# Optimization experiments

Measured on AMD Instinct MI355X. Metric: run time of the kernel, lower is better.

Reference implementation:

```python
import jax, jax.numpy as jnp
import numpy as np

B, L, E, H = 4, 2048, 512, 8
D = E // H
FACTOR = 5
U = min(FACTOR * int(np.ceil(np.log(L))), L)  # sample_k == n_top == 40


def setup_inputs() -> dict:
    key0 = jax.random.key(0)
    ks = jax.random.split(key0, 12)
    s = 0.02
    inp = {
        "query": jax.random.normal(ks[0], (B, L, E), jnp.float32),
        "key": jax.random.normal(ks[1], (B, L, E), jnp.float32),
        "value": jax.random.normal(ks[2], (B, L, E), jnp.float32),
        "index_sample": jax.random.randint(ks[3], (L, U), 0, L, jnp.int32),
    }
    for i, nm in enumerate(["q", "k", "v", "o"]):
        inp[f"W{nm}"] = jax.random.normal(ks[4 + i], (E, E), jnp.float32) * s
        inp[f"b{nm}"] = jnp.zeros((E,), jnp.float32)
    return inp


def reference(query, key, value, index_sample, Wq, bq, Wk, bk, Wv, bv, Wo, bo):
    # projections (nn.Linear: x @ W.T + b)
    q = (query @ Wq.T + bq).reshape(B, L, H, D).transpose(0, 2, 1, 3)  # [B,H,L,D]
    k = (key @ Wk.T + bk).reshape(B, L, H, D).transpose(0, 2, 1, 3)
    v = (value @ Wv.T + bv).reshape(B, L, H, D).transpose(0, 2, 1, 3)

    L_Q = L_K = L
    sample_k = index_sample.shape[1]
    n_top = min(sample_k, L_Q)

    # --- _prob_QK: sampled QK scores, note: NO 1/sqrt(D) scaling in source ---
    K_sample = k[:, :, index_sample, :]                      # [B,H,L_Q,sample_k,D]
    QK_sample = jnp.einsum('bhld,bhlsd->bhls', q, K_sample)  # [B,H,L_Q,sample_k]
    M = QK_sample.max(axis=-1) - QK_sample.sum(axis=-1) / L_K
    _, M_top = jax.lax.top_k(M, n_top)                       # [B,H,n_top]
    Q_reduce = jnp.take_along_axis(q, M_top[..., None], axis=2)  # [B,H,n_top,D]
    scores = jnp.einsum('bhud,bhkd->bhuk', Q_reduce, k)      # [B,H,n_top,L_K]

    # --- initial context (eval mode: mean of V) ---
    context = jnp.broadcast_to(v.mean(axis=2, keepdims=True), (B, H, L_Q, D))

    # --- update context at selected queries ---
    attn = jax.nn.softmax(scores, axis=-1)
    upd = jnp.einsum('bhuk,bhkd->bhud', attn, v)             # [B,H,n_top,D]
    bi = jnp.arange(B)[:, None, None]
    hi = jnp.arange(H)[None, :, None]
    context = context.at[bi, hi, M_top].set(upd)

    out = context.transpose(0, 2, 1, 3).reshape(B, L, E) @ Wo.T + bo
    return out
```

## Files before the change

### kernel.cpp

```cpp
#include <hip/hip_runtime.h>
#include <hip/hip_bf16.h>
#include <math.h>

constexpr int BB = 4;
constexpr int LL = 2048;
constexpr int EE = 512;
constexpr int HH = 8;
constexpr int DD = 64;
constexpr int UU = 40;
constexpr int NT = 40;
constexpr int NCH = 32;
constexpr int CK = 64;
constexpr int MVC = 16;
constexpr float NEG_INF = -3.0e38f;

typedef __attribute__((ext_vector_type(8))) short bf8_t;
typedef __attribute__((ext_vector_type(4))) float f4_t;

__device__ __forceinline__ void split2pair(float x0, float x1, uint& hp, uint& mp)
{
    uint xb0 = __float_as_uint(x0), xb1 = __float_as_uint(x1);
    uint hb0 = xb0 + 0x7fffu + ((xb0 >> 16) & 1u);
    uint hb1 = xb1 + 0x7fffu + ((xb1 >> 16) & 1u);
    hp = __builtin_amdgcn_perm(hb1, hb0, 0x07060302u);
    float r0 = x0 - __uint_as_float(hb0 & 0xffff0000u);
    float r1 = x1 - __uint_as_float(hb1 & 0xffff0000u);
    mp = __builtin_amdgcn_perm(__float_as_uint(r1), __float_as_uint(r0), 0x07060302u);
}

__device__ __forceinline__ void gload16(const void* g, void* l)
{
    __builtin_amdgcn_global_load_lds(
        (const __attribute__((address_space(1))) unsigned int*)g,
        (__attribute__((address_space(3))) unsigned int*)l, 16, 0, 0);
}

__device__ __forceinline__ int swz(int row, int c)
{
    return row * 64 + (((c ^ row ^ (row >> 2)) & 3) << 4);
}

__global__ __launch_bounds__(256) void wconv_kernel(
    const float* __restrict__ Wq, const float* __restrict__ Wk,
    const float* __restrict__ Wv, unsigned short* __restrict__ wcv)
{
    const int gi  = blockIdx.x * 256 + threadIdx.x;
    const int z   = gi >> 15;
    const int off = (gi & 32767) * 8;
    const float* W = (z == 0) ? Wq : (z == 1 ? Wk : Wv);
    float x[8];
    *(float4*)(x)     = *(const float4*)(W + off);
    *(float4*)(x + 4) = *(const float4*)(W + off + 4);
    uint hp[4], mp[4];
#pragma unroll
    for (int p = 0; p < 4; p++) split2pair(x[2 * p], x[2 * p + 1], hp[p], mp[p]);
    unsigned short* Wh = wcv + (size_t)z * 524288;
    *(uint4*)(Wh + off)          = make_uint4(hp[0], hp[1], hp[2], hp[3]);
    *(uint4*)(Wh + 262144 + off) = make_uint4(mp[0], mp[1], mp[2], mp[3]);
}

__global__ __launch_bounds__(256, 3) void proj_kernel(
    const float* __restrict__ Xq, const float* __restrict__ Xk, const float* __restrict__ Xv,
    const unsigned short* __restrict__ Wcv,
    const float* __restrict__ bq, const float* __restrict__ bk, const float* __restrict__ bv,
    float* __restrict__ Oq, float* __restrict__ Ok, float* __restrict__ Ov)
{
    const int bid = blockIdx.x;
    const int xg  = bid & 7;
    const int s   = bid >> 3;
    const int yz  = xg * 24 + (s >> 2);
    const int zi  = yz >> 6;
    const int yi  = yz & 63;
    const int m0  = yi * 128;
    const int n0  = (s & 3) * 128;

    const float* X; const float* bias; float* O;
    if (zi == 0)      { X = Xq; bias = bq; O = Oq; }
    else if (zi == 1) { X = Xk; bias = bk; O = Ok; }
    else              { X = Xv; bias = bv; O = Ov; }
    const unsigned short* Wh = Wcv + (size_t)zi * 524288;
    const unsigned short* Wm = Wh + 262144;

    __shared__ char ldsmem[49152];
    char* const LA = ldsmem;
    char* const LB = ldsmem + 16384;

    const int tid  = threadIdx.x;
    const int lane = tid & 63;
    const int wave = tid >> 6;

    const int srow  = tid >> 1;
    const int shalf = tid & 1;
    const int w0 = swz(srow, shalf * 2);
    const int w1 = swz(srow, shalf * 2 + 1);
    const float* Aptr = X + (size_t)(m0 + srow) * EE + shalf * 16;

    const int r0 = tid >> 2;
    const int r1 = 64 + r0;
    const int c0 = (tid & 3) ^ ((r0 ^ (r0 >> 2)) & 3);
    const int c1 = (tid & 3) ^ ((r1 ^ (r1 >> 2)) & 3);
    const unsigned short* bh0 = Wh + (size_t)(n0 + r0) * EE + c0 * 8;
    const unsigned short* bh1 = Wh + (size_t)(n0 + r1) * EE + c1 * 8;
    const unsigned short* bm0 = Wm + (size_t)(n0 + r0) * EE + c0 * 8;
    const unsigned short* bm1 = Wm + (size_t)(n0 + r1) * EE + c1 * 8;
    const int ldst = tid * 16;

    const int rxor = ((((lane >> 4) ^ lane ^ (lane >> 2)) & 3) << 4);
    const int arow = (wave >> 1) * 64 + (lane & 15);
    const int brow = (wave & 1) * 64 + (lane & 15);

    f4_t acc[4][4];
#pragma unroll
    for (int i = 0; i < 4; i++)
#pragma unroll
        for (int j = 0; j < 4; j++) acc[i][j] = (f4_t)0.0f;

    float fa[16];
#pragma unroll
    for (int q = 0; q < 4; q++)
        *(float4*)(fa + q * 4) = *(const float4*)(Aptr + q * 4);
    gload16(bh0, LB + ldst);
    gload16(bh1, LB + 4096 + ldst);
    gload16(bm0, LB + 8192 + ldst);
    gload16(bm1, LB + 12288 + ldst);

    int parity = 0;
#pragma unroll 2
    for (int kt = 0; kt < EE; kt += 32) {
        uint ahu[8], amu[8];
#pragma unroll
        for (int p = 0; p < 8; p++)
            split2pair(fa[2 * p], fa[2 * p + 1], ahu[p], amu[p]);

        __syncthreads();
        *(uint4*)(LA +    0 + w0) = make_uint4(ahu[0], ahu[1], ahu[2], ahu[3]);
        *(uint4*)(LA +    0 + w1) = make_uint4(ahu[4], ahu[5], ahu[6], ahu[7]);
        *(uint4*)(LA + 8192 + w0) = make_uint4(amu[0], amu[1], amu[2], amu[3]);
        *(uint4*)(LA + 8192 + w1) = make_uint4(amu[4], amu[5], amu[6], amu[7]);
        __syncthreads();

        if (kt + 32 < EE) {
            const int kn = kt + 32;
#pragma unroll
            for (int q = 0; q < 4; q++)
                *(float4*)(fa + q * 4) = *(const float4*)(Aptr + kn + q * 4);
            char* Bn = LB + (parity ^ 1) * 16384;
            gload16(bh0 + kn, Bn + ldst);
            gload16(bh1 + kn, Bn + 4096 + ldst);
            gload16(bm0 + kn, Bn + 8192 + ldst);
            gload16(bm1 + kn, Bn + 12288 + ldst);
        }

        char* const Bb = LB + parity * 16384;
        bf8_t af[4][2];
#pragma unroll
        for (int i = 0; i < 4; i++) {
            const int ro = (arow + i * 16) * 64 + rxor;
            af[i][0] = *(const bf8_t*)(LA +    0 + ro);
            af[i][1] = *(const bf8_t*)(LA + 8192 + ro);
        }
#pragma unroll
        for (int j = 0; j < 4; j++) {
            const int ro = (brow + j * 16) * 64 + rxor;
            bf8_t bh_ = *(const bf8_t*)(Bb +    0 + ro);
            bf8_t bm_ = *(const bf8_t*)(Bb + 8192 + ro);
#pragma unroll
            for (int i = 0; i < 4; i++) {
                f4_t c = acc[i][j];
                c = __builtin_amdgcn_mfma_f32_16x16x32_bf16(af[i][0], bh_, c, 0, 0, 0);
                c = __builtin_amdgcn_mfma_f32_16x16x32_bf16(af[i][0], bm_, c, 0, 0, 0);
                c = __builtin_amdgcn_mfma_f32_16x16x32_bf16(af[i][1], bh_, c, 0, 0, 0);
                acc[i][j] = c;
            }
        }
        parity ^= 1;
    }

#pragma unroll
    for (int j = 0; j < 4; j++) {
        const int n  = n0 + (wave & 1) * 64 + j * 16 + (lane & 15);
        const float bn = bias[n];
        const int h_ = n >> 6, d_ = n & 63;
#pragma unroll
        for (int i = 0; i < 4; i++) {
            const int mb = m0 + (wave >> 1) * 64 + i * 16 + ((lane >> 4) << 2);
#pragma unroll
            for (int r = 0; r < 4; r++) {
                const int m  = mb + r;
                const int b_ = m >> 11;
                const int l_ = m & (LL - 1);
                O[(((size_t)(b_ * HH + h_) * LL + l_) << 6) + d_] = acc[i][j][r] + bn;
            }
        }
    }
}

__global__ __launch_bounds__(256) void meanv_part_kernel(const float* __restrict__ v,
                                                         float* __restrict__ vpart)
{
    const int bh    = blockIdx.x & 31;
    const int chunk = blockIdx.x >> 5;
    const int d  = threadIdx.x & 63;
    const int wv = threadIdx.x >> 6;
    const float* base = v + ((size_t)bh * LL + chunk * 128 + wv * 32) * DD + d;
    float acc = 0.0f;
#pragma unroll
    for (int i = 0; i < 32; i++) acc += base[i * DD];
    __shared__ float red[4][DD];
    red[wv][d] = acc;
    __syncthreads();
    if (wv == 0)
        vpart[(size_t)(chunk * 32 + bh) * DD + d]
            = red[0][d] + red[1][d] + red[2][d] + red[3][d];
}

__global__ __launch_bounds__(64) void meanv_comb_kernel(const float* __restrict__ vpart,
                                                        float* __restrict__ mean_v)
{
    const int bh = blockIdx.x;
    const int d  = threadIdx.x;
    float s = 0.0f;
#pragma unroll
    for (int c = 0; c < MVC; c++) s += vpart[(size_t)(c * 32 + bh) * DD + d];
    mean_v[bh * DD + d] = s * (1.0f / (float)LL);
}

__global__ __launch_bounds__(256) void measure_kernel(const float* __restrict__ q,
                                                      const float* __restrict__ k,
                                                      const int* __restrict__ idx_sample,
                                                      float* __restrict__ M)
{
    int bh   = blockIdx.x & 31;
    int lc   = blockIdx.x >> 5;
    int lane = threadIdx.x & 63;
    int wv   = threadIdx.x >> 6;
    int l    = lc * 4 + wv;
    int s8   = lane >> 3;
    int c    = lane & 7;

    const float* qrow = q + ((size_t)bh * LL + l) * DD + c * 8;
    float4 q0 = *(const float4*)(qrow);
    float4 q1 = *(const float4*)(qrow + 4);

    const float* kbase = k + (size_t)bh * LL * DD;
    const int*   irow  = idx_sample + l * UU;

    float mx = NEG_INF, sum = 0.0f;
#pragma unroll
    for (int it = 0; it < UU; it += 8) {
        int ki = irow[it + s8];
        const float* krow = kbase + (size_t)ki * DD + c * 8;
        float4 k0 = *(const float4*)(krow);
        float4 k1 = *(const float4*)(krow + 4);
        float p = q0.x*k0.x + q0.y*k0.y + q0.z*k0.z + q0.w*k0.w
                + q1.x*k1.x + q1.y*k1.y + q1.z*k1.z + q1.w*k1.w;
        p += __shfl_xor(p, 1, 64);
        p += __shfl_xor(p, 2, 64);
        p += __shfl_xor(p, 4, 64);
        mx = fmaxf(mx, p);
        sum += p;
    }
    mx  = fmaxf(mx, __shfl_xor(mx, 8, 64));
    sum += __shfl_xor(sum, 8, 64);
    mx  = fmaxf(mx, __shfl_xor(mx, 16, 64));
    sum += __shfl_xor(sum, 16, 64);
    mx  = fmaxf(mx, __shfl_xor(mx, 32, 64));
    sum += __shfl_xor(sum, 32, 64);

    if (lane == 0) M[bh * LL + l] = mx - sum * (1.0f / (float)LL);
}

__global__ __launch_bounds__(64) void topk_kernel(const float* __restrict__ M,
                                                  int* __restrict__ top)
{
    const int bh   = blockIdx.x;
    const int lane = threadIdx.x;

    unsigned long long keys[32];
#pragma unroll
    for (int i = 0; i < 32; i++) {
        int idx = i * 64 + lane;
        uint u  = __float_as_uint(M[bh * LL + idx]);
        uint sv = (u & 0x80000000u) ? ~u : (u | 0x80000000u);
        keys[i] = ((unsigned long long)sv << 32) | (uint)(LL - 1 - idx);
    }
    unsigned long long lmax = 0ull;
#pragma unroll
    for (int i = 0; i < 32; i++) lmax = (keys[i] > lmax) ? keys[i] : lmax;

    for (int it = 0; it < NT; it++) {
        unsigned long long g = lmax;
#pragma unroll
        for (int off = 1; off < 64; off <<= 1) {
            unsigned long long o = __shfl_xor(g, off, 64);
            g = (o > g) ? o : g;
        }
        if (lane == 0) top[bh * NT + it] = LL - 1 - (int)(g & 0xffffffffu);
#pragma unroll
        for (int i = 0; i < 32; i++) if (keys[i] == g) keys[i] = 0ull;
        lmax = 0ull;
#pragma unroll
        for (int i = 0; i < 32; i++) lmax = (keys[i] > lmax) ? keys[i] : lmax;
    }
}

__global__ __launch_bounds__(256) void pv_kernel(const float* __restrict__ q,
                                                 const float* __restrict__ k,
                                                 const float* __restrict__ v,
                                                 const int* __restrict__ top,
                                                 float* __restrict__ mpart,
                                                 float* __restrict__ lpart,
                                                 float* __restrict__ accpart)
{
    const int bh    = blockIdx.x & 31;
    const int chunk = blockIdx.x >> 5;
    const int tid   = threadIdx.x;
    const int lane  = tid & 63, wv = tid >> 6;

    __shared__ float qs[NT][DD];
    __shared__ float sc[NT][CK + 4];

    for (int i = tid; i < NT * DD / 4; i += 256) {
        int u  = i >> 4;
        int d4 = (i & 15) * 4;
        int l  = top[bh * NT + u];
        *(float4*)&qs[u][d4] = *(const float4*)(q + ((size_t)bh * LL + l) * DD + d4);
    }
    __syncthreads();

    {
        const int key  = tid >> 2;
        const int dseg = tid & 3;
        const float* krow = k + ((size_t)bh * LL + chunk * CK + key) * DD + dseg * 16;
        float4 k0 = *(const float4*)(krow);
        float4 k1 = *(const float4*)(krow + 4);
        float4 k2 = *(const float4*)(krow + 8);
        float4 k3 = *(const float4*)(krow + 12);
#pragma unroll 8
        for (int u = 0; u < NT; u++) {
            const float* qrow = &qs[u][dseg * 16];
            float4 q0 = *(const float4*)(qrow);
            float4 q1 = *(const float4*)(qrow + 4);
            float4 q2 = *(const float4*)(qrow + 8);
            float4 q3 = *(const float4*)(qrow + 12);
            float p = k0.x*q0.x + k0.y*q0.y + k0.z*q0.z + k0.w*q0.w
                    + k1.x*q1.x + k1.y*q1.y + k1.z*q1.z + k1.w*q1.w
                    + k2.x*q2.x + k2.y*q2.y + k2.z*q2.z + k2.w*q2.w
                    + k3.x*q3.x + k3.y*q3.y + k3.z*q3.z + k3.w*q3.w;
            p += __shfl_xor(p, 1, 64);
            p += __shfl_xor(p, 2, 64);
            if (dseg == 0) sc[u][key] = p;
        }
    }
    __syncthreads();

#pragma unroll
    for (int i = 0; i < 10; i++) {
        const int u = wv * 10 + i;
        float val = sc[u][lane];
        float mx = val;
        mx = fmaxf(mx, __shfl_xor(mx, 1, 64));
        mx = fmaxf(mx, __shfl_xor(mx, 2, 64));
        mx = fmaxf(mx, __shfl_xor(mx, 4, 64));
        mx = fmaxf(mx, __shfl_xor(mx, 8, 64));
        mx = fmaxf(mx, __shfl_xor(mx, 16, 64));
        mx = fmaxf(mx, __shfl_xor(mx, 32, 64));
        float e = __expf(val - mx);
        sc[u][lane] = e;
        float s = e;
        s += __shfl_xor(s, 1, 64);
        s += __shfl_xor(s, 2, 64);
        s += __shfl_xor(s, 4, 64);
        s += __shfl_xor(s, 8, 64);
        s += __shfl_xor(s, 16, 64);
        s += __shfl_xor(s, 32, 64);
        if (lane == 0) {
            mpart[(bh * NCH + chunk) * NT + u] = mx;
            lpart[(bh * NCH + chunk) * NT + u] = s;
        }
    }
    __syncthreads();

    {
        float pacc[10];
#pragma unroll
        for (int i = 0; i < 10; i++) pacc[i] = 0.0f;
        const float* vbase = v + ((size_t)bh * LL + chunk * CK) * DD;
#pragma unroll 8
        for (int t = 0; t < CK; t++) {
            float vval = vbase[(size_t)t * DD + lane];
#pragma unroll
            for (int i = 0; i < 10; i++) pacc[i] += sc[wv * 10 + i][t] * vval;
        }
#pragma unroll
        for (int i = 0; i < 10; i++) {
            const int u = wv * 10 + i;
            accpart[(((size_t)(bh * NCH + chunk)) * NT + u) * 64 + lane] = pacc[i];
        }
    }
}

__global__ __launch_bounds__(256) void base_kernel(const float* __restrict__ mean_v,
                                                   const float* __restrict__ Wo,
                                                   const float* __restrict__ bo,
                                                   float* __restrict__ base)
{
    int lane = threadIdx.x & 63, wv = threadIdx.x >> 6;
    int be = blockIdx.x * 4 + wv;
    int b  = be >> 9;
    int e  = be & (EE - 1);
    const float* mrow = mean_v + b * EE;
    const float* wrow = Wo + (size_t)e * EE;
    float acc = 0.0f;
#pragma unroll
    for (int j = 0; j < 8; j++) acc += mrow[lane + j * 64] * wrow[lane + j * 64];
#pragma unroll
    for (int off = 32; off > 0; off >>= 1) acc += __shfl_down(acc, off, 64);
    if (lane == 0) base[be] = acc + bo[e];
}

__global__ __launch_bounds__(256) void bcast_kernel(const float* __restrict__ base,
                                                    float* __restrict__ out)
{
    size_t fi = ((size_t)blockIdx.x * 256 + threadIdx.x) * 4;
    int b  = (int)(fi >> 20);
    int e4 = (int)(fi & (EE - 1));
    float4 val = *(const float4*)(base + b * EE + e4);
    *(float4*)(out + fi) = val;
}

__global__ __launch_bounds__(256) void corr_kernel(const float* __restrict__ accpart,
                                                   const float* __restrict__ lpart,
                                                   const float* __restrict__ mpart,
                                                   const float* __restrict__ mean_v,
                                                   const int* __restrict__ top,
                                                   const float* __restrict__ Wo,
                                                   float* __restrict__ out)
{
    const int bh  = blockIdx.x & 31;
    const int ec  = blockIdx.x >> 5;
    const int h   = bh & (HH - 1);
    const int b   = bh >> 3;
    const int tid = threadIdx.x;

    __shared__ float delta[NT][DD + 1];
    __shared__ float wot[128][DD + 1];
    __shared__ int   ltab[NT];

    {
        const int ug = tid >> 6;
        const int d  = tid & 63;
        for (int u = ug; u < NT; u += 4) {
            const float* mp = mpart + (size_t)bh * NCH * NT + u;
            const float* lp = lpart + (size_t)bh * NCH * NT + u;
            float m = NEG_INF;
#pragma unroll 8
            for (int c = 0; c < NCH; c++) m = fmaxf(m, mp[c * NT]);
            float den = 0.0f, num = 0.0f;
#pragma unroll 8
            for (int c = 0; c < NCH; c++) {
                float f = __expf(mp[c * NT] - m);
                den += lp[c * NT] * f;
                num += accpart[(((size_t)(bh * NCH + c)) * NT + u) * 64 + d] * f;
            }
            delta[u][d] = num / den - mean_v[bh * DD + d];
        }
    }
    if (tid < NT) ltab[tid] = top[bh * NT + tid];

    const int e0 = ec * 128;
#pragma unroll
    for (int p = 0; p < 8; p++) {
        const int r  = p * 16 + (tid >> 4);
        const int c4 = (tid & 15) * 4;
        *(float4*)&wot[r][c4] = *(const float4*)(Wo + (size_t)(e0 + r) * EE + h * DD + c4);
    }
    __syncthreads();

    const int el = tid >> 1;
    const int u0 = (tid & 1) * 20;
    float* orowbase = out + (size_t)b * LL * EE + e0 + el;
#pragma unroll 4
    for (int uu = 0; uu < 20; uu++) {
        const int u = u0 + uu;
        float acc = 0.0f;
#pragma unroll
        for (int d = 0; d < DD; d++) acc += delta[u][d] * wot[el][d];
        atomicAdd(orowbase + (size_t)ltab[u] * EE, acc);
    }
}

extern "C" void kernel_launch(void* const* d_in, const int* in_sizes, int n_in,
                              void* d_out, int out_size, void* d_ws, size_t ws_size,
                              hipStream_t stream)
{
    const float* query = (const float*)d_in[0];
    const float* key   = (const float*)d_in[1];
    const float* value = (const float*)d_in[2];
    const int*   idxs  = (const int*)d_in[3];
    const float* Wq = (const float*)d_in[4];
    const float* bq = (const float*)d_in[5];
    const float* Wk = (const float*)d_in[6];
    const float* bk = (const float*)d_in[7];
    const float* Wv = (const float*)d_in[8];
    const float* bv = (const float*)d_in[9];
    const float* Wo = (const float*)d_in[10];
    const float* bo = (const float*)d_in[11];
    float* out = (float*)d_out;

    char* ws = (char*)d_ws;
    size_t off = 0;
    const size_t qkv_bytes = (size_t)BB * HH * LL * DD * sizeof(float);
    float* q_ws = (float*)(ws + off); off += qkv_bytes;
    float* k_ws = (float*)(ws + off); off += qkv_bytes;
    float* v_ws = (float*)(ws + off); off += qkv_bytes;
    float* M_ws    = (float*)(ws + off); off += (size_t)BB * HH * LL * sizeof(float);
    int*   top_ws  = (int*)(ws + off);   off += (size_t)BB * HH * NT * sizeof(int);
    float* mean_ws = (float*)(ws + off); off += (size_t)BB * HH * DD * sizeof(float);
    float* vpart_ws = (float*)(ws + off); off += (size_t)BB * HH * MVC * DD * sizeof(float);
    float* mpart_ws = (float*)(ws + off); off += (size_t)BB * HH * NCH * NT * sizeof(float);
    float* lpart_ws = (float*)(ws + off); off += (size_t)BB * HH * NCH * NT * sizeof(float);
    float* accpart_ws = (float*)(ws + off); off += (size_t)BB * HH * NCH * NT * DD * sizeof(float);
    float* base_ws = (float*)(ws + off); off += (size_t)BB * EE * sizeof(float);

    unsigned short* wcv_ws = (unsigned short*)accpart_ws;

    wconv_kernel<<<384, 256, 0, stream>>>(Wq, Wk, Wv, wcv_ws);
    proj_kernel<<<768, 256, 0, stream>>>(query, key, value, wcv_ws, bq, bk, bv,
                                         q_ws, k_ws, v_ws);
    meanv_part_kernel<<<BB * HH * MVC, 256, 0, stream>>>(v_ws, vpart_ws);
    meanv_comb_kernel<<<BB * HH, 64, 0, stream>>>(vpart_ws, mean_ws);
    measure_kernel<<<(LL / 4) * 32, 256, 0, stream>>>(q_ws, k_ws, idxs, M_ws);
    topk_kernel<<<BB * HH, 64, 0, stream>>>(M_ws, top_ws);
    pv_kernel<<<BB * HH * NCH, 256, 0, stream>>>(q_ws, k_ws, v_ws, top_ws,
                                                 mpart_ws, lpart_ws, accpart_ws);
    base_kernel<<<(BB * EE) / 4, 256, 0, stream>>>(mean_ws, Wo, bo, base_ws);
    bcast_kernel<<<(BB * LL * EE) / (256 * 4), 256, 0, stream>>>(base_ws, out);
    corr_kernel<<<128, 256, 0, stream>>>(accpart_ws, lpart_ws, mpart_ws,
                                         mean_ws, top_ws, Wo, out);
}
```

Before: 312.8 us.

## Split correction into parallel delta-combine kernel and register-tiled output projection

After: 272.0 us. 13.0% less time.

```diff
diff --git a/kernel.cpp b/kernel.cpp
--- a/kernel.cpp
+++ b/kernel.cpp
@@ -429,64 +429,79 @@
     *(float4*)(out + fi) = val;
 }
 
-__global__ __launch_bounds__(256) void corr_kernel(const float* __restrict__ accpart,
+__global__ __launch_bounds__(64) void delta_kernel(const float* __restrict__ accpart,
                                                    const float* __restrict__ lpart,
                                                    const float* __restrict__ mpart,
                                                    const float* __restrict__ mean_v,
-                                                   const int* __restrict__ top,
-                                                   const float* __restrict__ Wo,
-                                                   float* __restrict__ out)
+                                                   float* __restrict__ delta_ws)
+{
+    const int bhu = blockIdx.x;
+    const int bh  = bhu / NT;
+    const int u   = bhu % NT;
+    const int d   = threadIdx.x;
+
+    const float* mp = mpart + (size_t)bh * NCH * NT + u;
+    const float* lp = lpart + (size_t)bh * NCH * NT + u;
+    const float* ap = accpart + ((size_t)bh * NCH * NT + u) * 64 + d;
+
+    float m = NEG_INF;
+#pragma unroll
+    for (int c = 0; c < NCH; c++) m = fmaxf(m, mp[c * NT]);
+    float den = 0.0f, num = 0.0f;
+#pragma unroll
+    for (int c = 0; c < NCH; c++) {
+        float f = __expf(mp[c * NT] - m);
+        den += lp[c * NT] * f;
+        num += ap[(size_t)c * NT * 64] * f;
+    }
+    delta_ws[(size_t)bhu * 64 + d] = num / den - mean_v[bh * DD + d];
+}
+
+__global__ __launch_bounds__(256) void corr2_kernel(const float* __restrict__ delta_ws,
+                                                    const int* __restrict__ top,
+                                                    const float* __restrict__ Wo,
+                                                    float* __restrict__ out)
 {
     const int bh  = blockIdx.x & 31;
     const int ec  = blockIdx.x >> 5;
     const int h   = bh & (HH - 1);
     const int b   = bh >> 3;
     const int tid = threadIdx.x;
-
-    __shared__ float delta[NT][DD + 1];
-    __shared__ float wot[128][DD + 1];
-    __shared__ int   ltab[NT];
-
-    {
-        const int ug = tid >> 6;
-        const int d  = tid & 63;
-        for (int u = ug; u < NT; u += 4) {
-            const float* mp = mpart + (size_t)bh * NCH * NT + u;
-            const float* lp = lpart + (size_t)bh * NCH * NT + u;
-            float m = NEG_INF;
-#pragma unroll 8
-            for (int c = 0; c < NCH; c++) m = fmaxf(m, mp[c * NT]);
-            float den = 0.0f, num = 0.0f;
-#pragma unroll 8
-            for (int c = 0; c < NCH; c++) {
-                float f = __expf(mp[c * NT] - m);
-                den += lp[c * NT] * f;
-                num += accpart[(((size_t)(bh * NCH + c)) * NT + u) * 64 + d] * f;
-            }
-            delta[u][d] = num / den - mean_v[bh * DD + d];
-        }
+    const int lane = tid & 63;
+    const int wv   = tid >> 6;
+
+    __shared__ alignas(16) float dl[NT][DD];
+    __shared__ int ltab[NT];
+
+    for (int i = tid; i < NT * DD / 4; i += 256) {
+        const int u  = i >> 4;
+        const int d4 = (i & 15) * 4;
+        *(float4*)&dl[u][d4] = *(const float4*)(delta_ws + ((size_t)(bh * NT + u)) * 64 + d4);
     }
     if (tid < NT) ltab[tid] = top[bh * NT + tid];
 
-    const int e0 = ec * 128;
-#pragma unroll
-    for (int p = 0; p < 8; p++) {
-        const int r  = p * 16 + (tid >> 4);
-        const int c4 = (tid & 15) * 4;
-        *(float4*)&wot[r][c4] = *(const float4*)(Wo + (size_t)(e0 + r) * EE + h * DD + c4);
-    }
+    const int e = ec * 64 + lane;
+    const float* wrow = Wo + (size_t)e * EE + h * DD;
+    float4 wo[16];
+#pragma unroll
+    for (int j = 0; j < 16; j++) wo[j] = *(const float4*)(wrow + j * 4);
+
     __syncthreads();
 
-    const int el = tid >> 1;
-    const int u0 = (tid & 1) * 20;
-    float* orowbase = out + (size_t)b * LL * EE + e0 + el;
-#pragma unroll 4
-    for (int uu = 0; uu < 20; uu++) {
-        const int u = u0 + uu;
+    float* obase = out + (size_t)b * LL * EE + e;
+#pragma unroll
+    for (int uu = 0; uu < 10; uu++) {
+        const int u = wv * 10 + uu;
         float acc = 0.0f;
 #pragma unroll
-        for (int d = 0; d < DD; d++) acc += delta[u][d] * wot[el][d];
-        atomicAdd(orowbase + (size_t)ltab[u] * EE, acc);
+        for (int j = 0; j < 16; j++) {
+            float4 dv = *(const float4*)&dl[u][j * 4];
+            acc = fmaf(dv.x, wo[j].x, acc);
+            acc = fmaf(dv.y, wo[j].y, acc);
+            acc = fmaf(dv.z, wo[j].z, acc);
+            acc = fmaf(dv.w, wo[j].w, acc);
+        }
+        atomicAdd(obase + (size_t)ltab[u] * EE, acc);
     }
 }
 
@@ -522,6 +537,7 @@
     float* lpart_ws = (float*)(ws + off); off += (size_t)BB * HH * NCH * NT * sizeof(float);
     float* accpart_ws = (float*)(ws + off); off += (size_t)BB * HH * NCH * NT * DD * sizeof(float);
     float* base_ws = (float*)(ws + off); off += (size_t)BB * EE * sizeof(float);
+    float* delta_ws = (float*)(ws + off); off += (size_t)BB * HH * NT * DD * sizeof(float);
 
     unsigned short* wcv_ws = (unsigned short*)accpart_ws;
 
@@ -536,6 +552,7 @@
                                                  mpart_ws, lpart_ws, accpart_ws);
     base_kernel<<<(BB * EE) / 4, 256, 0, stream>>>(mean_ws, Wo, bo, base_ws);
     bcast_kernel<<<(BB * LL * EE) / (256 * 4), 256, 0, stream>>>(base_ws, out);
-    corr_kernel<<<128, 256, 0, stream>>>(accpart_ws, lpart_ws, mpart_ws,
-                                         mean_ws, top_ws, Wo, out);
-}
+    delta_kernel<<<BB * HH * NT, 64, 0, stream>>>(accpart_ws, lpart_ws, mpart_ws,
+                                                  mean_ws, delta_ws);
+    corr2_kernel<<<256, 256, 0, stream>>>(delta_ws, top_ws, Wo, out);
+}
```
